# Kernel optimization log

Measured on AMD Instinct MI355X. Metric: run time of the kernel, lower is better.

## Reference

```python
import jax, jax.numpy as jnp
import numpy as np

N_NODES = 50000
N_EDGES = 800000
IN_CH = 128
HID = 128


def _linear_params(key, fan_in, fan_out):
    kw, kb = jax.random.split(key)
    bound = 1.0 / np.sqrt(fan_in)
    W = jax.random.uniform(kw, (fan_in, fan_out), jnp.float32, -bound, bound)
    b = jax.random.uniform(kb, (fan_out,), jnp.float32, -bound, bound)
    return W, b


def setup_inputs() -> dict:
    key = jax.random.key(0)
    ks = jax.random.split(key, 11)
    x = jax.random.normal(ks[0], (N_NODES, IN_CH), jnp.float32)
    guidance_features = jax.random.normal(ks[1], (N_NODES, HID), jnp.float32)
    edge_index = jax.random.randint(ks[2], (2, N_EDGES), 0, N_NODES, jnp.int64)
    node_W, node_b = _linear_params(ks[3], IN_CH, HID)
    nbr_W, nbr_b = _linear_params(ks[4], IN_CH, HID)
    gud_W, gud_b = _linear_params(ks[5], HID, HID)
    enc_W, enc_b = _linear_params(ks[6], 3 * HID, HID)
    vp_W1, vp_b1 = _linear_params(ks[7], HID, HID // 2)
    vp_W2, vp_b2 = _linear_params(ks[8], HID // 2, 1)
    pol_W1, pol_b1 = _linear_params(ks[9], HID, HID)
    pol_W2, pol_b2 = _linear_params(ks[10], HID, 1)
    return dict(x=x, edge_index=edge_index, guidance_features=guidance_features,
                node_W=node_W, node_b=node_b, nbr_W=nbr_W, nbr_b=nbr_b,
                gud_W=gud_W, gud_b=gud_b, enc_W=enc_W, enc_b=enc_b,
                vp_W1=vp_W1, vp_b1=vp_b1, vp_W2=vp_W2, vp_b2=vp_b2,
                pol_W1=pol_W1, pol_b1=pol_b1, pol_W2=pol_W2, pol_b2=pol_b2)


def reference(x, edge_index, guidance_features,
              node_W, node_b, nbr_W, nbr_b, gud_W, gud_b,
              enc_W, enc_b, vp_W1, vp_b1, vp_W2, vp_b2,
              pol_W1, pol_b1, pol_W2, pol_b2):
    row, col = edge_index[0], edge_index[1]
    # Edge-wise gathers feeding three linear transforms -> [E, 3*HID] state
    node_feat = x[row] @ node_W + node_b            # [E, HID]
    nbr_feat = x[col] @ nbr_W + nbr_b               # [E, HID]
    gud_feat = guidance_features[col] @ gud_W + gud_b  # [E, HID]
    state = jnp.concatenate([node_feat, nbr_feat, gud_feat], axis=1)
    # state_encoder (eval mode: dropout = identity)
    enc = jax.nn.relu(state @ enc_W + enc_b)        # [E, HID]
    # value_predictor
    value_preds = jax.nn.relu(enc @ vp_W1 + vp_b1) @ vp_W2 + vp_b2  # [E, 1]
    # policy_net
    action_probs = jax.nn.sigmoid(
        jax.nn.relu(enc @ pol_W1 + pol_b1) @ pol_W2 + pol_b2)      # [E, 1]
    actions = (action_probs > 0.5).astype(x.dtype)  # eval-mode actions
    value_loss = jnp.zeros((), x.dtype)             # eval mode, labels=None
    return value_preds, action_probs, actions, value_loss
```

## Files before the change

### kernel.cpp

```cpp
#include <hip/hip_runtime.h>
#include <math.h>

#define N_NODES 50000
#define N_EDGES 800000

typedef __attribute__((ext_vector_type(8))) short short8_t;
typedef __attribute__((ext_vector_type(4))) float float4_t;

union U8 { short8_t v; unsigned short u[8]; };

__device__ __forceinline__ unsigned short bf16_rn(float f) {
    unsigned u = __float_as_uint(f);
    u += 0x7fffu + ((u >> 16) & 1u);
    return (unsigned short)(u >> 16);
}
__device__ __forceinline__ float bf2f(unsigned short h) {
    return __uint_as_float((unsigned)h << 16);
}
__device__ __forceinline__ void split3(float f, unsigned short& s0,
                                       unsigned short& s1, unsigned short& s2) {
    s0 = bf16_rn(f);  float r = f - bf2f(s0);
    s1 = bf16_rn(r);  r -= bf2f(s1);
    s2 = bf16_rn(r);
}
__device__ __forceinline__ void split3t(float f, unsigned short& s0,
                                        unsigned short& s1, unsigned short& s2) {
    unsigned u = __float_as_uint(f);
    s0 = (unsigned short)(u >> 16);
    float r = f - bf2f(s0);
    unsigned v = __float_as_uint(r);
    s1 = (unsigned short)(v >> 16);
    float r2 = r - bf2f(s1);
    s2 = bf16_rn(r2);
}


__global__ __launch_bounds__(256) void prep_kernel(
    const float* __restrict__ node_W, const float* __restrict__ node_b,
    const float* __restrict__ nbr_W,  const float* __restrict__ nbr_b,
    const float* __restrict__ gud_W,  const float* __restrict__ gud_b,
    const float* __restrict__ enc_W,  const float* __restrict__ enc_b,
    const float* __restrict__ vp_W1,  const float* __restrict__ vp_b1,
    const float* __restrict__ vp_W2,  const float* __restrict__ pol_W1,
    const float* __restrict__ pol_b1, const float* __restrict__ pol_W2,
    unsigned short* __restrict__ BTn0, unsigned short* __restrict__ BTn1,
    unsigned short* __restrict__ BTn2,
    unsigned short* __restrict__ BTg0, unsigned short* __restrict__ BTg1,
    unsigned short* __restrict__ BTg2,
    unsigned short* __restrict__ BTw0, unsigned short* __restrict__ BTw1,
    unsigned short* __restrict__ BTw2,
    float* __restrict__ cb, float* __restrict__ b1c, float* __restrict__ W2c,
    int* __restrict__ flags)
{
    const int k = blockIdx.x;
    const int j = threadIdx.x;
    if (j < 128) {
        float a = 0.f, b = 0.f;
        #pragma unroll 4
        for (int m = 0; m < 128; ++m) {
            a = fmaf(node_W[k * 128 + m], enc_W[m * 128 + j], a);
            b = fmaf(gud_W [k * 128 + m], enc_W[(256 + m) * 128 + j], b);
        }
        size_t i1 = (size_t)j * 128 + k;
        split3(a, BTn0[i1], BTn1[i1], BTn2[i1]);
        split3(b, BTg0[i1], BTg1[i1], BTg2[i1]);
    } else {
        const int n = j - 128;
        float a = 0.f;
        #pragma unroll 4
        for (int m = 0; m < 128; ++m)
            a = fmaf(nbr_W[k * 128 + m], enc_W[(128 + m) * 128 + n], a);
        size_t i2 = (size_t)(128 + n) * 128 + k;
        split3(a, BTn0[i2], BTn1[i2], BTn2[i2]);
    }
    if (j < 192) {
        float wv = (j < 64) ? vp_W1[k * 64 + j] : pol_W1[k * 128 + (j - 64)];
        size_t iw = (size_t)j * 128 + k;
        split3(wv, BTw0[iw], BTw1[iw], BTw2[iw]);
    }
    if (k == 0) {
        if (j < 128) {
            float cc = enc_b[j];
            for (int m = 0; m < 128; ++m) {
                cc = fmaf(node_b[m], enc_W[m * 128 + j], cc);
                cc = fmaf(nbr_b [m], enc_W[(128 + m) * 128 + j], cc);
                cc = fmaf(gud_b [m], enc_W[(256 + m) * 128 + j], cc);
            }
            cb[j] = cc;
        }
        if (j < 192) {
            b1c[j] = (j < 64) ? vp_b1[j] : pol_b1[j - 64];
            W2c[j] = (j < 64) ? vp_W2[j] : pol_W2[j - 64];
        }
        if (j < 64) {
            const int l = j, li = l & 15, lq = l >> 4;
            U8 A, B;
            #pragma unroll
            for (int u = 0; u < 8; ++u) { A.u[u] = 0; B.u[u] = 0; }
            if (lq == 0) {
                A.u[0] = bf16_rn((float)(li + 1));
                A.u[1] = bf16_rn(1.0f);
                B.u[0] = bf16_rn(1.0f);
                B.u[1] = bf16_rn((float)(100 * (li + 1)));
            }
            float4_t d = (float4_t){0.f, 0.f, 0.f, 0.f};
            d = __builtin_amdgcn_mfma_f32_16x16x32_bf16(A.v, B.v, d, 0, 0, 0);
            if (l == 17) {
                flags[0] = (fabsf(d[2] - 702.f) < 1.0f) ? 1 : 0;
            }
        }
    }
}

__global__ __launch_bounds__(256, 3) void node_kernel(
    const float* __restrict__ x, const float* __restrict__ g,
    const unsigned short* __restrict__ BTn0, const unsigned short* __restrict__ BTn1,
    const unsigned short* __restrict__ BTn2,
    const unsigned short* __restrict__ BTg0, const unsigned short* __restrict__ BTg1,
    const unsigned short* __restrict__ BTg2,
    const float* __restrict__ cb, const int* __restrict__ flags,
    float* __restrict__ P, float* __restrict__ Q)
{
    __shared__ unsigned short a0s[4 * 64 * 8];
    __shared__ unsigned short a1s[4 * 64 * 8];
    __shared__ unsigned short a2s[4 * 64 * 8];
    const int t = threadIdx.x;
    const int w = t >> 6, lane = t & 63;
    const int i16 = lane & 15, q = lane >> 4;
    const int base = blockIdx.x * 64;
    const int swap = flags[0];
    const int el = t >> 2, hh = t & 3;
    int nodeL = base + el; if (nodeL > N_NODES - 1) nodeL = N_NODES - 1;
    const float* xrow = x + (size_t)nodeL * 128 + hh * 8;
    const float* grow = g + (size_t)nodeL * 128 + hh * 8;

    float4_t acc[4][4];
    #pragma unroll
    for (int mt = 0; mt < 4; ++mt)
        #pragma unroll
        for (int nt = 0; nt < 4; ++nt) acc[mt][nt] = (float4_t){0.f, 0.f, 0.f, 0.f};

    float4 pv0 = *(const float4*)(xrow);
    float4 pv1 = *(const float4*)(xrow + 4);

    for (int kc = 0; kc < 8; ++kc) {
        U8 s0, s1, s2;
        {
            float e[8] = {pv0.x, pv0.y, pv0.z, pv0.w, pv1.x, pv1.y, pv1.z, pv1.w};
            #pragma unroll
            for (int u = 0; u < 8; ++u) split3t(e[u], s0.u[u], s1.u[u], s2.u[u]);
        }
        __syncthreads();
        {
            size_t off = ((size_t)hh * 64 + el) * 8;
            *(short8_t*)(a0s + off) = s0.v;
            *(short8_t*)(a1s + off) = s1.v;
            *(short8_t*)(a2s + off) = s2.v;
        }
        __syncthreads();
        if (kc < 7) {
            const float* nsrc = (kc + 1 < 4) ? (xrow + (kc + 1) * 32)
                                             : (grow + (kc + 1 - 4) * 32);
            pv0 = *(const float4*)(nsrc);
            pv1 = *(const float4*)(nsrc + 4);
        }
        if (kc < 4) {
            short8_t b0[4], b1v[4], b2v[4];
            #pragma unroll
            for (int ntl = 0; ntl < 4; ++ntl) {
                int ntg = w + ntl * 4;
                size_t roff = ((size_t)(ntg * 16 + i16)) * 128 + kc * 32 + q * 8;
                b0[ntl]  = *(const short8_t*)(BTn0 + roff);
                b1v[ntl] = *(const short8_t*)(BTn1 + roff);
                b2v[ntl] = *(const short8_t*)(BTn2 + roff);
            }
            #pragma unroll
            for (int mt = 0; mt < 4; ++mt) {
                size_t aoff = ((size_t)q * 64 + mt * 16 + i16) * 8;
                short8_t a0 = *(const short8_t*)(a0s + aoff);
                short8_t a1 = *(const short8_t*)(a1s + aoff);
                short8_t a2 = *(const short8_t*)(a2s + aoff);
                #pragma unroll
                for (int ntl = 0; ntl < 4; ++ntl) {
                    float4_t c = acc[mt][ntl];
                    c = __builtin_amdgcn_mfma_f32_16x16x32_bf16(a0, b0[ntl],  c, 0, 0, 0);
                    c = __builtin_amdgcn_mfma_f32_16x16x32_bf16(a0, b1v[ntl], c, 0, 0, 0);
                    c = __builtin_amdgcn_mfma_f32_16x16x32_bf16(a1, b0[ntl],  c, 0, 0, 0);
                    c = __builtin_amdgcn_mfma_f32_16x16x32_bf16(a0, b2v[ntl], c, 0, 0, 0);
                    c = __builtin_amdgcn_mfma_f32_16x16x32_bf16(a1, b1v[ntl], c, 0, 0, 0);
                    c = __builtin_amdgcn_mfma_f32_16x16x32_bf16(a2, b0[ntl],  c, 0, 0, 0);
                    acc[mt][ntl] = c;
                }
            }
        } else {
            short8_t b0[2], b1v[2], b2v[2];
            #pragma unroll
            for (int ntl = 0; ntl < 2; ++ntl) {
                int ntg = w + (ntl + 2) * 4;
                size_t roff = ((size_t)((ntg - 8) * 16 + i16)) * 128 + (kc - 4) * 32 + q * 8;
                b0[ntl]  = *(const short8_t*)(BTg0 + roff);
                b1v[ntl] = *(const short8_t*)(BTg1 + roff);
                b2v[ntl] = *(const short8_t*)(BTg2 + roff);
            }
            #pragma unroll
            for (int mt = 0; mt < 4; ++mt) {
                size_t aoff = ((size_t)q * 64 + mt * 16 + i16) * 8;
                short8_t a0 = *(const short8_t*)(a0s + aoff);
                short8_t a1 = *(const short8_t*)(a1s + aoff);
                short8_t a2 = *(const short8_t*)(a2s + aoff);
                #pragma unroll
                for (int ntl = 0; ntl < 2; ++ntl) {
                    float4_t c = acc[mt][ntl + 2];
                    c = __builtin_amdgcn_mfma_f32_16x16x32_bf16(a0, b0[ntl],  c, 0, 0, 0);
                    c = __builtin_amdgcn_mfma_f32_16x16x32_bf16(a0, b1v[ntl], c, 0, 0, 0);
                    c = __builtin_amdgcn_mfma_f32_16x16x32_bf16(a1, b0[ntl],  c, 0, 0, 0);
                    c = __builtin_amdgcn_mfma_f32_16x16x32_bf16(a0, b2v[ntl], c, 0, 0, 0);
                    c = __builtin_amdgcn_mfma_f32_16x16x32_bf16(a1, b1v[ntl], c, 0, 0, 0);
                    c = __builtin_amdgcn_mfma_f32_16x16x32_bf16(a2, b0[ntl],  c, 0, 0, 0);
                    acc[mt][ntl + 2] = c;
                }
            }
        }
    }

    if (!swap) {
        #pragma unroll
        for (int mt = 0; mt < 4; ++mt)
            #pragma unroll
            for (int ntl = 0; ntl < 4; ++ntl) {
                int ntg = w + ntl * 4;
                int chan = ntg * 16 + i16;
                bool isP = (ntg < 8);
                float bias = isP ? cb[chan] : 0.f;
                #pragma unroll
                for (int r = 0; r < 4; ++r) {
                    int node = base + mt * 16 + q * 4 + r;
                    if (node < N_NODES) {
                        if (isP) P[(size_t)node * 128 + chan] = acc[mt][ntl][r] + bias;
                        else     Q[(size_t)node * 128 + (chan - 128)] = acc[mt][ntl][r];
                    }
                }
            }
    } else {
        #pragma unroll
        for (int mt = 0; mt < 4; ++mt) {
            int node = base + mt * 16 + i16;
            if (node < N_NODES) {
                #pragma unroll
                for (int ntl = 0; ntl < 4; ++ntl) {
                    int ntg = w + ntl * 4;
                    int chanb = ntg * 16 + q * 4;
                    bool isP = (ntg < 8);
                    float4 vv;
                    vv.x = acc[mt][ntl][0] + (isP ? cb[chanb + 0] : 0.f);
                    vv.y = acc[mt][ntl][1] + (isP ? cb[chanb + 1] : 0.f);
                    vv.z = acc[mt][ntl][2] + (isP ? cb[chanb + 2] : 0.f);
                    vv.w = acc[mt][ntl][3] + (isP ? cb[chanb + 3] : 0.f);
                    if (isP) *(float4*)(P + (size_t)node * 128 + chanb) = vv;
                    else     *(float4*)(Q + (size_t)node * 128 + chanb - 128) = vv;
                }
            }
        }
    }
}

__global__ __launch_bounds__(256, 2) void edge_kernel(
    const int* __restrict__ ei,
    const float* __restrict__ P, const float* __restrict__ Q,
    const unsigned short* __restrict__ BTw0, const unsigned short* __restrict__ BTw1,
    const unsigned short* __restrict__ BTw2,
    const float* __restrict__ b1c, const float* __restrict__ W2c,
    const float* __restrict__ vp_b2, const float* __restrict__ pol_b2,
    const int* __restrict__ flags,
    float* __restrict__ out)
{
    __shared__ unsigned short enc0[4 * 128 * 8];
    __shared__ unsigned short enc1[4 * 128 * 8];
    __shared__ unsigned short enc2[4 * 128 * 8];
    __shared__ float vpart[512], ppart[512];

    const int t = threadIdx.x;
    const int w = t >> 6, lane = t & 63;
    const int i16 = lane & 15, q = lane >> 4;
    const int e0 = blockIdx.x * 128;
    const int ntg0 = w * 3;
    const int el = t >> 1, hh = t & 1;
    const int swap = flags[0];

    const int rowI = ei[e0 + el];
    const int colI = ei[N_EDGES + e0 + el];
    const float* Pp = P + (size_t)rowI * 128 + hh * 16;
    const float* Qp = Q + (size_t)colI * 128 + hh * 16;

    float4_t acc[8][3];
    #pragma unroll
    for (int mt = 0; mt < 8; ++mt)
        #pragma unroll
        for (int nt = 0; nt < 3; ++nt) acc[mt][nt] = (float4_t){0.f, 0.f, 0.f, 0.f};

    float4 pv[4], qv[4];
    #pragma unroll
    for (int i = 0; i < 4; ++i) {
        pv[i] = *(const float4*)(Pp + i * 4);
        qv[i] = *(const float4*)(Qp + i * 4);
    }

    for (int kc = 0; kc < 4; ++kc) {
        U8 g0[2], g1[2], g2[2];
        #pragma unroll
        for (int i = 0; i < 4; ++i) {
            float ev[4] = {fmaxf(pv[i].x + qv[i].x, 0.f), fmaxf(pv[i].y + qv[i].y, 0.f),
                           fmaxf(pv[i].z + qv[i].z, 0.f), fmaxf(pv[i].w + qv[i].w, 0.f)};
            #pragma unroll
            for (int u = 0; u < 4; ++u) {
                int idx = i * 4 + u;
                split3t(ev[u], g0[idx >> 3].u[idx & 7], g1[idx >> 3].u[idx & 7],
                        g2[idx >> 3].u[idx & 7]);
            }
        }
        __syncthreads();
        #pragma unroll
        for (int hb = 0; hb < 2; ++hb) {
            size_t off = ((size_t)(2 * hh + hb) * 128 + el) * 8;
            *(short8_t*)(enc0 + off) = g0[hb].v;
            *(short8_t*)(enc1 + off) = g1[hb].v;
            *(short8_t*)(enc2 + off) = g2[hb].v;
        }
        __syncthreads();
        if (kc < 3) {
            #pragma unroll
            for (int i = 0; i < 4; ++i) {
                pv[i] = *(const float4*)(Pp + (kc + 1) * 32 + i * 4);
                qv[i] = *(const float4*)(Qp + (kc + 1) * 32 + i * 4);
            }
        }
        short8_t b0[3], b1f[3], b2f[3];
        #pragma unroll
        for (int ntl = 0; ntl < 3; ++ntl) {
            size_t roff = ((size_t)((ntg0 + ntl) * 16 + i16)) * 128 + kc * 32 + q * 8;
            b0[ntl]  = *(const short8_t*)(BTw0 + roff);
            b1f[ntl] = *(const short8_t*)(BTw1 + roff);
            b2f[ntl] = *(const short8_t*)(BTw2 + roff);
        }
        #pragma unroll
        for (int mt = 0; mt < 8; ++mt) {
            size_t aoff = ((size_t)q * 128 + mt * 16 + i16) * 8;
            short8_t a0 = *(const short8_t*)(enc0 + aoff);
            short8_t a1 = *(const short8_t*)(enc1 + aoff);
            short8_t a2 = *(const short8_t*)(enc2 + aoff);
            #pragma unroll
            for (int ntl = 0; ntl < 3; ++ntl) {
                float4_t c = acc[mt][ntl];
                c = __builtin_amdgcn_mfma_f32_16x16x32_bf16(a0, b0[ntl],  c, 0, 0, 0);
                c = __builtin_amdgcn_mfma_f32_16x16x32_bf16(a0, b1f[ntl], c, 0, 0, 0);
                c = __builtin_amdgcn_mfma_f32_16x16x32_bf16(a1, b0[ntl],  c, 0, 0, 0);
                c = __builtin_amdgcn_mfma_f32_16x16x32_bf16(a0, b2f[ntl], c, 0, 0, 0);
                c = __builtin_amdgcn_mfma_f32_16x16x32_bf16(a1, b1f[ntl], c, 0, 0, 0);
                c = __builtin_amdgcn_mfma_f32_16x16x32_bf16(a2, b0[ntl],  c, 0, 0, 0);
                acc[mt][ntl] = c;
            }
        }
    }

    if (!swap) {
        #pragma unroll
        for (int mt = 0; mt < 8; ++mt) {
            float vs[4] = {0.f, 0.f, 0.f, 0.f}, ps[4] = {0.f, 0.f, 0.f, 0.f};
            #pragma unroll
            for (int ntl = 0; ntl < 3; ++ntl) {
                int ntg = ntg0 + ntl;
                int n = ntg * 16 + i16;
                float b1s = b1c[n], w2s = W2c[n];
                bool isv = (ntg < 4);
                #pragma unroll
                for (int r = 0; r < 4; ++r) {
                    float hv = fmaxf(acc[mt][ntl][r] + b1s, 0.f) * w2s;
                    if (isv) vs[r] += hv; else ps[r] += hv;
                }
            }
            #pragma unroll
            for (int off = 1; off < 16; off <<= 1)
                #pragma unroll
                for (int r = 0; r < 4; ++r) {
                    vs[r] += __shfl_xor(vs[r], off, 64);
                    ps[r] += __shfl_xor(ps[r], off, 64);
                }
            if (i16 == 0)
                #pragma unroll
                for (int r = 0; r < 4; ++r) {
                    int eidx = mt * 16 + q * 4 + r;
                    vpart[w * 128 + eidx] = vs[r];
                    ppart[w * 128 + eidx] = ps[r];
                }
        }
    } else {
        #pragma unroll
        for (int mt = 0; mt < 8; ++mt) {
            float v = 0.f, p = 0.f;
            #pragma unroll
            for (int ntl = 0; ntl < 3; ++ntl) {
                int ntg = ntg0 + ntl;
                bool isv = (ntg < 4);
                #pragma unroll
                for (int r = 0; r < 4; ++r) {
                    int n = ntg * 16 + q * 4 + r;
                    float hv = fmaxf(acc[mt][ntl][r] + b1c[n], 0.f) * W2c[n];
                    if (isv) v += hv; else p += hv;
                }
            }
            v += __shfl_xor(v, 16, 64); v += __shfl_xor(v, 32, 64);
            p += __shfl_xor(p, 16, 64); p += __shfl_xor(p, 32, 64);
            if (q == 0) {
                int eidx = mt * 16 + i16;
                vpart[w * 128 + eidx] = v;
                ppart[w * 128 + eidx] = p;
            }
        }
    }
    __syncthreads();
    if (t < 128) {
        float v  = vpart[t] + vpart[128 + t] + vpart[256 + t] + vpart[384 + t] + vp_b2[0];
        float pl = ppart[t] + ppart[128 + t] + ppart[256 + t] + ppart[384 + t] + pol_b2[0];
        float prob = 1.0f / (1.0f + expf(-pl));
        int e = e0 + t;
        out[e] = v;
        out[N_EDGES + e] = prob;
        out[2 * N_EDGES + e] = (prob > 0.5f) ? 1.0f : 0.0f;
    }
    if (blockIdx.x == 0 && t == 0) out[3 * N_EDGES] = 0.0f;
}

extern "C" void kernel_launch(void* const* d_in, const int* in_sizes, int n_in,
                              void* d_out, int out_size, void* d_ws, size_t ws_size,
                              hipStream_t stream) {
    const float* x      = (const float*)d_in[0];
    const int*   ei     = (const int*)  d_in[1];
    const float* gf     = (const float*)d_in[2];
    const float* node_W = (const float*)d_in[3];
    const float* node_b = (const float*)d_in[4];
    const float* nbr_W  = (const float*)d_in[5];
    const float* nbr_b  = (const float*)d_in[6];
    const float* gud_W  = (const float*)d_in[7];
    const float* gud_b  = (const float*)d_in[8];
    const float* enc_W  = (const float*)d_in[9];
    const float* enc_b  = (const float*)d_in[10];
    const float* vp_W1  = (const float*)d_in[11];
    const float* vp_b1  = (const float*)d_in[12];
    const float* vp_W2  = (const float*)d_in[13];
    const float* vp_b2  = (const float*)d_in[14];
    const float* pol_W1 = (const float*)d_in[15];
    const float* pol_b1 = (const float*)d_in[16];
    const float* pol_W2 = (const float*)d_in[17];
    const float* pol_b2 = (const float*)d_in[18];
    float* out = (float*)d_out;

    unsigned char* wsb = (unsigned char*)d_ws;
    unsigned short* BTn0 = (unsigned short*)(wsb + 0);
    unsigned short* BTn1 = (unsigned short*)(wsb + 65536);
    unsigned short* BTn2 = (unsigned short*)(wsb + 131072);
    unsigned short* BTg0 = (unsigned short*)(wsb + 196608);
    unsigned short* BTg1 = (unsigned short*)(wsb + 229376);
    unsigned short* BTg2 = (unsigned short*)(wsb + 262144);
    unsigned short* BTw0 = (unsigned short*)(wsb + 294912);
    unsigned short* BTw1 = (unsigned short*)(wsb + 344064);
    unsigned short* BTw2 = (unsigned short*)(wsb + 393216);
    float* cb   = (float*)(wsb + 442368);
    float* b1c  = (float*)(wsb + 442880);
    float* W2c  = (float*)(wsb + 443648);
    int*   flags= (int*)  (wsb + 444416);
    float* Pd   = (float*)(wsb + 444480);
    float* Qd   = Pd + (size_t)N_NODES * 128;

    prep_kernel<<<dim3(128), dim3(256), 0, stream>>>(
        node_W, node_b, nbr_W, nbr_b, gud_W, gud_b, enc_W, enc_b,
        vp_W1, vp_b1, vp_W2, pol_W1, pol_b1, pol_W2,
        BTn0, BTn1, BTn2, BTg0, BTg1, BTg2, BTw0, BTw1, BTw2,
        cb, b1c, W2c, flags);

    node_kernel<<<dim3((N_NODES + 63) / 64), dim3(256), 0, stream>>>(
        x, gf, BTn0, BTn1, BTn2, BTg0, BTg1, BTg2, cb, flags, Pd, Qd);

    edge_kernel<<<dim3(N_EDGES / 128), dim3(256), 0, stream>>>(
        ei, Pd, Qd, BTw0, BTw1, BTw2, b1c, W2c, vp_b2, pol_b2, flags, out);
}
```

Before: 515.7 us.

## Double-buffer edge encoding LDS tiles and software-pipeline weight fragment loads

Doubles the shared-memory encoding buffers so the k-chunk loop runs as a fully unrolled ping-pong pipeline. The next chunk's relu/bf16-split staging is written to the alternate buffer while MFMAs consume the current one, which cuts the two barriers per chunk to one. Weight B-fragments for the next chunk are loaded into a second register set before the current MFMA phase. This raises shared memory per block (about 24KB more) and register pressure, which may threaten the 2-blocks-per-CU occupancy target.

New measurement: 543.7 us. +5.4%, slower.

```diff
diff --git a/kernel.cpp b/kernel.cpp
--- a/kernel.cpp
+++ b/kernel.cpp
@@ -264,6 +264,74 @@
     }
 }
 
+#define STAGE(BUF)                                                              \
+    {                                                                           \
+        U8 g0[2], g1[2], g2[2];                                                 \
+        _Pragma("unroll")                                                       \
+        for (int i = 0; i < 4; ++i) {                                           \
+            float ev[4] = {fmaxf(pv[i].x + qv[i].x, 0.f),                       \
+                           fmaxf(pv[i].y + qv[i].y, 0.f),                       \
+                           fmaxf(pv[i].z + qv[i].z, 0.f),                       \
+                           fmaxf(pv[i].w + qv[i].w, 0.f)};                      \
+            _Pragma("unroll")                                                   \
+            for (int u = 0; u < 4; ++u) {                                       \
+                int idx = i * 4 + u;                                            \
+                split3t(ev[u], g0[idx >> 3].u[idx & 7], g1[idx >> 3].u[idx & 7],\
+                        g2[idx >> 3].u[idx & 7]);                               \
+            }                                                                   \
+        }                                                                       \
+        _Pragma("unroll")                                                       \
+        for (int hb = 0; hb < 2; ++hb) {                                        \
+            size_t off = ((size_t)(2 * hh + hb) * 128 + el) * 8;                \
+            *(short8_t*)(enc0[BUF] + off) = g0[hb].v;                           \
+            *(short8_t*)(enc1[BUF] + off) = g1[hb].v;                           \
+            *(short8_t*)(enc2[BUF] + off) = g2[hb].v;                           \
+        }                                                                       \
+    }
+
+#define LOADB(KC, D0, D1, D2)                                                   \
+    {                                                                           \
+        _Pragma("unroll")                                                       \
+        for (int ntl = 0; ntl < 3; ++ntl) {                                     \
+            size_t roff = ((size_t)((ntg0 + ntl) * 16 + i16)) * 128             \
+                          + (KC) * 32 + q * 8;                                  \
+            D0[ntl] = *(const short8_t*)(BTw0 + roff);                          \
+            D1[ntl] = *(const short8_t*)(BTw1 + roff);                          \
+            D2[ntl] = *(const short8_t*)(BTw2 + roff);                          \
+        }                                                                       \
+    }
+
+#define PREFETCH_PQ(KC)                                                         \
+    {                                                                           \
+        _Pragma("unroll")                                                       \
+        for (int i = 0; i < 4; ++i) {                                           \
+            pv[i] = *(const float4*)(Pp + ((KC) + 1) * 32 + i * 4);             \
+            qv[i] = *(const float4*)(Qp + ((KC) + 1) * 32 + i * 4);             \
+        }                                                                       \
+    }
+
+#define MFMA_PHASE(BUF, B0, B1, B2)                                             \
+    {                                                                           \
+        _Pragma("unroll")                                                       \
+        for (int mt = 0; mt < 8; ++mt) {                                        \
+            size_t aoff = ((size_t)q * 128 + mt * 16 + i16) * 8;                \
+            short8_t a0 = *(const short8_t*)(enc0[BUF] + aoff);                 \
+            short8_t a1 = *(const short8_t*)(enc1[BUF] + aoff);                 \
+            short8_t a2 = *(const short8_t*)(enc2[BUF] + aoff);                 \
+            _Pragma("unroll")                                                   \
+            for (int ntl = 0; ntl < 3; ++ntl) {                                 \
+                float4_t c = acc[mt][ntl];                                      \
+                c = __builtin_amdgcn_mfma_f32_16x16x32_bf16(a0, B0[ntl], c, 0, 0, 0); \
+                c = __builtin_amdgcn_mfma_f32_16x16x32_bf16(a0, B1[ntl], c, 0, 0, 0); \
+                c = __builtin_amdgcn_mfma_f32_16x16x32_bf16(a1, B0[ntl], c, 0, 0, 0); \
+                c = __builtin_amdgcn_mfma_f32_16x16x32_bf16(a0, B2[ntl], c, 0, 0, 0); \
+                c = __builtin_amdgcn_mfma_f32_16x16x32_bf16(a1, B1[ntl], c, 0, 0, 0); \
+                c = __builtin_amdgcn_mfma_f32_16x16x32_bf16(a2, B0[ntl], c, 0, 0, 0); \
+                acc[mt][ntl] = c;                                               \
+            }                                                                   \
+        }                                                                       \
+    }
+
 __global__ __launch_bounds__(256, 2) void edge_kernel(
     const int* __restrict__ ei,
     const float* __restrict__ P, const float* __restrict__ Q,
@@ -274,9 +342,9 @@
     const int* __restrict__ flags,
     float* __restrict__ out)
 {
-    __shared__ unsigned short enc0[4 * 128 * 8];
-    __shared__ unsigned short enc1[4 * 128 * 8];
-    __shared__ unsigned short enc2[4 * 128 * 8];
+    __shared__ unsigned short enc0[2][4 * 128 * 8];
+    __shared__ unsigned short enc1[2][4 * 128 * 8];
+    __shared__ unsigned short enc2[2][4 * 128 * 8];
     __shared__ float vpart[512], ppart[512];
 
     const int t = threadIdx.x;
@@ -304,63 +372,27 @@
         pv[i] = *(const float4*)(Pp + i * 4);
         qv[i] = *(const float4*)(Qp + i * 4);
     }
-
-    for (int kc = 0; kc < 4; ++kc) {
-        U8 g0[2], g1[2], g2[2];
-        #pragma unroll
-        for (int i = 0; i < 4; ++i) {
-            float ev[4] = {fmaxf(pv[i].x + qv[i].x, 0.f), fmaxf(pv[i].y + qv[i].y, 0.f),
-                           fmaxf(pv[i].z + qv[i].z, 0.f), fmaxf(pv[i].w + qv[i].w, 0.f)};
-            #pragma unroll
-            for (int u = 0; u < 4; ++u) {
-                int idx = i * 4 + u;
-                split3t(ev[u], g0[idx >> 3].u[idx & 7], g1[idx >> 3].u[idx & 7],
-                        g2[idx >> 3].u[idx & 7]);
-            }
-        }
-        __syncthreads();
-        #pragma unroll
-        for (int hb = 0; hb < 2; ++hb) {
-            size_t off = ((size_t)(2 * hh + hb) * 128 + el) * 8;
-            *(short8_t*)(enc0 + off) = g0[hb].v;
-            *(short8_t*)(enc1 + off) = g1[hb].v;
-            *(short8_t*)(enc2 + off) = g2[hb].v;
-        }
-        __syncthreads();
-        if (kc < 3) {
-            #pragma unroll
-            for (int i = 0; i < 4; ++i) {
-                pv[i] = *(const float4*)(Pp + (kc + 1) * 32 + i * 4);
-                qv[i] = *(const float4*)(Qp + (kc + 1) * 32 + i * 4);
-            }
-        }
-        short8_t b0[3], b1f[3], b2f[3];
-        #pragma unroll
-        for (int ntl = 0; ntl < 3; ++ntl) {
-            size_t roff = ((size_t)((ntg0 + ntl) * 16 + i16)) * 128 + kc * 32 + q * 8;
-            b0[ntl]  = *(const short8_t*)(BTw0 + roff);
-            b1f[ntl] = *(const short8_t*)(BTw1 + roff);
-            b2f[ntl] = *(const short8_t*)(BTw2 + roff);
-        }
-        #pragma unroll
-        for (int mt = 0; mt < 8; ++mt) {
-            size_t aoff = ((size_t)q * 128 + mt * 16 + i16) * 8;
-            short8_t a0 = *(const short8_t*)(enc0 + aoff);
-            short8_t a1 = *(const short8_t*)(enc1 + aoff);
-            short8_t a2 = *(const short8_t*)(enc2 + aoff);
-            #pragma unroll
-            for (int ntl = 0; ntl < 3; ++ntl) {
-                float4_t c = acc[mt][ntl];
-                c = __builtin_amdgcn_mfma_f32_16x16x32_bf16(a0, b0[ntl],  c, 0, 0, 0);
-                c = __builtin_amdgcn_mfma_f32_16x16x32_bf16(a0, b1f[ntl], c, 0, 0, 0);
-                c = __builtin_amdgcn_mfma_f32_16x16x32_bf16(a1, b0[ntl],  c, 0, 0, 0);
-                c = __builtin_amdgcn_mfma_f32_16x16x32_bf16(a0, b2f[ntl], c, 0, 0, 0);
-                c = __builtin_amdgcn_mfma_f32_16x16x32_bf16(a1, b1f[ntl], c, 0, 0, 0);
-                c = __builtin_amdgcn_mfma_f32_16x16x32_bf16(a2, b0[ntl],  c, 0, 0, 0);
-                acc[mt][ntl] = c;
-            }
-        }
-    }
+    short8_t bA0[3], bA1[3], bA2[3], bB0[3], bB1[3], bB2[3];
+    LOADB(0, bA0, bA1, bA2);
+
+    STAGE(0);
+    __syncthreads();
+    PREFETCH_PQ(0);
+    LOADB(1, bB0, bB1, bB2);
+    MFMA_PHASE(0, bA0, bA1, bA2);
+    STAGE(1);
+    __syncthreads();
+    PREFETCH_PQ(1);
+    LOADB(2, bA0, bA1, bA2);
+    MFMA_PHASE(1, bB0, bB1, bB2);
+    STAGE(0);
+    __syncthreads();
+    PREFETCH_PQ(2);
+    LOADB(3, bB0, bB1, bB2);
+    MFMA_PHASE(0, bA0, bA1, bA2);
+    STAGE(1);
+    __syncthreads();
+    MFMA_PHASE(1, bB0, bB1, bB2);
 
     if (!swap) {
         #pragma unroll
```
